# Kernel optimization log

Measured on AMD Instinct MI355X. Metric: run time of the kernel, lower is better.

Reference implementation:

```python
import jax, jax.numpy as jnp
import numpy as np

N_NODES = 100000
NUM_FEATURES = 512
HIDDEN = 128
OUT = 2
N_EDGES = 1600000


def setup_inputs() -> dict:
    key = jax.random.key(0)
    k_x, k_e, k_w1, k_b1, k_w2, k_b2 = jax.random.split(key, 6)
    x = jax.random.normal(k_x, (N_NODES, NUM_FEATURES), dtype=jnp.float32)
    edge_index = jax.random.randint(k_e, (2, N_EDGES), 0, N_NODES, dtype=jnp.int64)
    # GCNConv weight (Glorot-style scale) and bias
    w1 = jax.random.normal(k_w1, (NUM_FEATURES, HIDDEN), dtype=jnp.float32) / np.sqrt(NUM_FEATURES)
    b1 = jnp.zeros((HIDDEN,), dtype=jnp.float32)
    # nn.Linear weight/bias
    w2 = jax.random.normal(k_w2, (HIDDEN, OUT), dtype=jnp.float32) / np.sqrt(HIDDEN)
    b2 = jnp.zeros((OUT,), dtype=jnp.float32)
    return {"x": x, "w1": w1, "b1": b1, "w2": w2, "b2": b2, "edge_index": edge_index}


def _gcn_conv(x, edge_index, w, b, num_nodes):
    """PyG GCNConv: h = D^{-1/2} (A+I) D^{-1/2} (x @ w) + b."""
    h = x @ w  # [N, hidden] -- transform before propagate (PyG order)
    loops = jnp.arange(num_nodes, dtype=edge_index.dtype)
    src = jnp.concatenate([edge_index[0], loops])  # [E+N]
    dst = jnp.concatenate([edge_index[1], loops])
    # symmetric normalization: deg computed over destination (col) incl. self-loops
    deg = jnp.zeros((num_nodes,), dtype=h.dtype).at[dst].add(1.0)
    dinv = jax.lax.rsqrt(deg)  # deg >= 1 thanks to self-loops
    norm = dinv[src] * dinv[dst]  # [E+N]
    msg = h[src] * norm[:, None]  # gather + scale, [E+N, hidden]
    out = jax.ops.segment_sum(msg, dst, num_segments=num_nodes)  # scatter-add
    return out + b


def reference(x, w1, b1, w2, b2, edge_index):
    h = _gcn_conv(x, edge_index, w1, b1, N_NODES)  # [N, hidden]
    return h @ w2 + b2  # [N, out]
```

## Files before the change

### kernel.cpp

```cpp
#include <hip/hip_runtime.h>

constexpr int N_NODES = 100000;
constexpr int N_FEAT  = 512;
constexpr int N_EDGES = 1600000;

constexpr float FXS = 1048576.0f;
constexpr float FXB = 32.0f;

constexpr int BSH   = 8;
constexpr int BINW  = 1 << BSH;
constexpr int NBINS = (N_NODES + BINW - 1) >> BSH;
constexpr int BCAP  = 5120;
constexpr int NBB   = 128;
constexpr int CHUNK = N_EDGES / NBB;
constexpr int NRB   = 2048;

typedef float vfloat4 __attribute__((ext_vector_type(4)));

constexpr int WS_W    = 0;
constexpr int WS_C    = 1024;
constexpr int WS_CUR  = 1056;
constexpr int WS_DEG  = WS_CUR + 512;
constexpr int WS_DINV = WS_DEG + N_NODES;
constexpr int WS_G    = WS_DINV + N_NODES;
constexpr int WS_BINS = WS_G + 2 * N_NODES;

__global__ void k_prep(const float* __restrict__ w1, const float* __restrict__ w2,
                       const float* __restrict__ b1, const float* __restrict__ b2,
                       float* __restrict__ ws) {
    int i = blockIdx.x * blockDim.x + threadIdx.x;
    if (i < NBINS) reinterpret_cast<int*>(ws + WS_CUR)[i] = 0;
    if (i < N_FEAT) {
        float a0 = 0.f, a1 = 0.f;
        for (int m = 0; m < 128; ++m) {
            float w = w1[i * 128 + m];
            a0 += w * w2[m * 2 + 0];
            a1 += w * w2[m * 2 + 1];
        }
        ws[WS_W + i] = a0;
        ws[WS_W + 512 + i] = a1;
        if (i < 2) {
            float s = b2[i];
            for (int m = 0; m < 128; ++m) s += b1[m] * w2[m * 2 + i];
            ws[WS_C + i] = s;
        }
    }
}

__global__ __launch_bounds__(256) void k_fused(
    const float* __restrict__ x, float* __restrict__ ws,
    const int* __restrict__ src, const int* __restrict__ dst,
    float2* __restrict__ g) {
    int b = blockIdx.x;
    if (b < NBB) {
        __shared__ int cnt[NBINS];
        __shared__ int offs[NBINS];
        __shared__ int cur2[NBINS];
        int tid = threadIdx.x;
        for (int i = tid; i < NBINS; i += 256) { cnt[i] = 0; cur2[i] = 0; }
        __syncthreads();
        int base = b * CHUNK;
        for (int e = base + tid; e < base + CHUNK; e += 256)
            atomicAdd(&cnt[dst[e] >> BSH], 1);
        __syncthreads();
        int* gcur = reinterpret_cast<int*>(ws + WS_CUR);
        for (int i = tid; i < NBINS; i += 256) {
            int c = cnt[i];
            int pos = c ? atomicAdd(&gcur[i], c) : 0;
            offs[i] = i * BCAP + pos;
        }
        __syncthreads();
        unsigned int* bins = reinterpret_cast<unsigned int*>(ws + WS_BINS);
        for (int e = base + tid; e < base + CHUNK; e += 256) {
            int d = dst[e], s = src[e];
            int bin = d >> BSH;
            int r = atomicAdd(&cur2[bin], 1);
            bins[offs[bin] + r] = (unsigned int)s | ((unsigned int)(d & (BINW - 1)) << 17);
        }
        return;
    }
    int rb = b - NBB;
    const vfloat4* W0q = reinterpret_cast<const vfloat4*>(ws + WS_W);
    const vfloat4* W1q = reinterpret_cast<const vfloat4*>(ws + WS_W + 512);
    int lane = threadIdx.x & 63;
    int wave = threadIdx.x >> 6;

    vfloat4 w0a = W0q[lane], w0b = W0q[64 + lane];
    vfloat4 w1a = W1q[lane], w1b = W1q[64 + lane];

    int wid = rb * 4 + wave;
    int nw  = NRB * 4;
    constexpr int NPAIR = N_NODES / 2;
    for (int p = wid; p < NPAIR; p += nw) {
        int row0 = p * 2;
        const vfloat4* xq0 = reinterpret_cast<const vfloat4*>(x + (size_t)row0 * N_FEAT);
        const vfloat4* xq1 = xq0 + 128;
        vfloat4 xa = __builtin_nontemporal_load(&xq0[lane]);
        vfloat4 xb = __builtin_nontemporal_load(&xq0[64 + lane]);
        vfloat4 ya = __builtin_nontemporal_load(&xq1[lane]);
        vfloat4 yb = __builtin_nontemporal_load(&xq1[64 + lane]);
        float a0 = xa.x*w0a.x + xa.y*w0a.y + xa.z*w0a.z + xa.w*w0a.w
                 + xb.x*w0b.x + xb.y*w0b.y + xb.z*w0b.z + xb.w*w0b.w;
        float a1 = xa.x*w1a.x + xa.y*w1a.y + xa.z*w1a.z + xa.w*w1a.w
                 + xb.x*w1b.x + xb.y*w1b.y + xb.z*w1b.z + xb.w*w1b.w;
        float b0 = ya.x*w0a.x + ya.y*w0a.y + ya.z*w0a.z + ya.w*w0a.w
                 + yb.x*w0b.x + yb.y*w0b.y + yb.z*w0b.z + yb.w*w0b.w;
        float b1v= ya.x*w1a.x + ya.y*w1a.y + ya.z*w1a.z + ya.w*w1a.w
                 + yb.x*w1b.x + yb.y*w1b.y + yb.z*w1b.z + yb.w*w1b.w;
        #pragma unroll
        for (int off = 32; off >= 1; off >>= 1) {
            a0 += __shfl_down(a0, off);
            a1 += __shfl_down(a1, off);
            b0 += __shfl_down(b0, off);
            b1v+= __shfl_down(b1v, off);
        }
        if (lane == 0) {
            g[row0]     = make_float2(a0, a1);
            g[row0 + 1] = make_float2(b0, b1v);
        }
    }
}

__global__ __launch_bounds__(256) void k_deg(float* __restrict__ ws) {
    int b = blockIdx.x;
    const int* gcur = reinterpret_cast<const int*>(ws + WS_CUR);
    const unsigned int* bins = reinterpret_cast<const unsigned int*>(ws + WS_BINS) + b * BCAP;
    int n = min(gcur[b], BCAP);
    __shared__ int cnt[BINW];
    cnt[threadIdx.x] = 0;
    __syncthreads();
    for (int i = threadIdx.x; i < n; i += 256)
        atomicAdd(&cnt[bins[i] >> 17], 1);
    __syncthreads();
    int d = (b << BSH) + threadIdx.x;
    if (d < N_NODES) {
        int dg = cnt[threadIdx.x] + 1;
        reinterpret_cast<int*>(ws + WS_DEG)[d] = dg;
        ws[WS_DINV + d] = rsqrtf((float)dg);
    }
}

__global__ __launch_bounds__(256) void k_pass2(float* __restrict__ ws,
                                               float2* __restrict__ out) {
    int b = blockIdx.x;
    const int* gcur = reinterpret_cast<const int*>(ws + WS_CUR);
    const unsigned int* bins = reinterpret_cast<const unsigned int*>(ws + WS_BINS) + b * BCAP;
    const int* deg = reinterpret_cast<const int*>(ws + WS_DEG);
    const float* dinv = ws + WS_DINV;
    const float2* g = reinterpret_cast<const float2*>(ws + WS_G);
    int n = min(gcur[b], BCAP);
    __shared__ unsigned long long acc[BINW];
    acc[threadIdx.x] = 0ull;
    __syncthreads();
    for (int i = threadIdx.x; i < n; i += 256) {
        unsigned int p = bins[i];
        int s  = (int)(p & 0x1FFFFu);
        int ld = (int)(p >> 17);
        float2 gv = g[s];
        float di = dinv[s];
        unsigned int lo = (unsigned int)__float2int_rn((gv.x * di + FXB) * FXS);
        unsigned int hi = (unsigned int)__float2int_rn((gv.y * di + FXB) * FXS);
        atomicAdd(&acc[ld], ((unsigned long long)hi << 32) | (unsigned long long)lo);
    }
    __syncthreads();
    int d = (b << BSH) + threadIdx.x;
    if (d < N_NODES) {
        unsigned long long a = acc[threadIdx.x];
        long long cnt = (long long)(deg[d] - 1);
        long long bias = cnt << 25;
        long long lo = (long long)(a & 0xFFFFFFFFull) - bias;
        long long hi = (long long)(a >> 32) - bias;
        float di = dinv[d];
        float2 gv = g[d];
        float s0 = (float)lo * (1.0f / FXS) + gv.x * di;
        float s1 = (float)hi * (1.0f / FXS) + gv.y * di;
        out[d] = make_float2(di * s0 + ws[WS_C + 0], di * s1 + ws[WS_C + 1]);
    }
}

extern "C" void kernel_launch(void* const* d_in, const int* in_sizes, int n_in,
                              void* d_out, int out_size, void* d_ws, size_t ws_size,
                              hipStream_t stream) {
    const float* x  = (const float*)d_in[0];
    const float* w1 = (const float*)d_in[1];
    const float* b1 = (const float*)d_in[2];
    const float* w2 = (const float*)d_in[3];
    const float* b2 = (const float*)d_in[4];
    const int*   ei = (const int*)d_in[5];
    float* ws = (float*)d_ws;

    float2* g = (float2*)(ws + WS_G);

    k_prep<<<2, 256, 0, stream>>>(w1, w2, b1, b2, ws);
    k_fused<<<NBB + NRB, 256, 0, stream>>>(x, ws, ei, ei + N_EDGES, g);
    k_deg<<<NBINS, 256, 0, stream>>>(ws);
    k_pass2<<<NBINS, 256, 0, stream>>>(ws, (float2*)d_out);
}
```

Baseline: 90.66 us.

## Fold degree pass into binning blocks via grid barrier; restructure x-projection to 4 rows per wave

The separate degree kernel is removed. The 128 binning blocks now sync through a global atomic counter and then compute degree and dinv for their share of bins, which saves one kernel launch. The x @ W projection now has each wave handle 4 rows, with 16 lanes per row and 8 vector loads per lane. This cuts the shuffle reduction from 6 to 4 steps and gives each lane more loads in flight. The spin barrier depends on all 128 binning blocks being resident at the same time, which adds a risk of deadlock. The row-block count is also lowered.

```diff
diff --git a/kernel.cpp b/kernel.cpp
--- a/kernel.cpp
+++ b/kernel.cpp
@@ -13,7 +13,8 @@
 constexpr int BCAP  = 5120;
 constexpr int NBB   = 128;
 constexpr int CHUNK = N_EDGES / NBB;
-constexpr int NRB   = 2048;
+constexpr int NRB   = 1920;
+constexpr int GRID  = NBB + NRB;
 
 typedef float vfloat4 __attribute__((ext_vector_type(4)));
 
@@ -25,11 +26,13 @@
 constexpr int WS_G    = WS_DINV + N_NODES;
 constexpr int WS_BINS = WS_G + 2 * N_NODES;
 
+static_assert(N_NODES % 4 == 0, "");
+
 __global__ void k_prep(const float* __restrict__ w1, const float* __restrict__ w2,
                        const float* __restrict__ b1, const float* __restrict__ b2,
                        float* __restrict__ ws) {
     int i = blockIdx.x * blockDim.x + threadIdx.x;
-    if (i < NBINS) reinterpret_cast<int*>(ws + WS_CUR)[i] = 0;
+    if (i < NBINS + 1) reinterpret_cast<int*>(ws + WS_CUR)[i] = 0;
     if (i < N_FEAT) {
         float a0 = 0.f, a1 = 0.f;
         for (int m = 0; m < 128; ++m) {
@@ -47,10 +50,9 @@
     }
 }
 
-__global__ __launch_bounds__(256) void k_fused(
+__global__ __launch_bounds__(256) void k_main(
     const float* __restrict__ x, float* __restrict__ ws,
-    const int* __restrict__ src, const int* __restrict__ dst,
-    float2* __restrict__ g) {
+    const int* __restrict__ src, const int* __restrict__ dst) {
     int b = blockIdx.x;
     if (b < NBB) {
         __shared__ int cnt[NBINS];
@@ -77,66 +79,73 @@
             int r = atomicAdd(&cur2[bin], 1);
             bins[offs[bin] + r] = (unsigned int)s | ((unsigned int)(d & (BINW - 1)) << 17);
         }
+        __threadfence();
+        __syncthreads();
+        int* flag = gcur + NBINS;
+        if (tid == 0) {
+            __hip_atomic_fetch_add(flag, 1, __ATOMIC_ACQ_REL, __HIP_MEMORY_SCOPE_AGENT);
+            while (__hip_atomic_load(flag, __ATOMIC_ACQUIRE, __HIP_MEMORY_SCOPE_AGENT) < NBB)
+                __builtin_amdgcn_s_sleep(2);
+        }
+        __syncthreads();
+        __threadfence();
+        int* degp = reinterpret_cast<int*>(ws + WS_DEG);
+        for (int bin = b; bin < NBINS; bin += NBB) {
+            int n = __hip_atomic_load(&gcur[bin], __ATOMIC_RELAXED, __HIP_MEMORY_SCOPE_AGENT);
+            n = min(n, BCAP);
+            if (tid < BINW) cnt[tid] = 0;
+            __syncthreads();
+            const unsigned int* bb = bins + bin * BCAP;
+            for (int i = tid; i < n; i += 256)
+                atomicAdd(&cnt[bb[i] >> 17], 1);
+            __syncthreads();
+            int d = (bin << BSH) + tid;
+            if (tid < BINW && d < N_NODES) {
+                int dg = cnt[tid] + 1;
+                degp[d] = dg;
+                ws[WS_DINV + d] = rsqrtf((float)dg);
+            }
+            __syncthreads();
+        }
         return;
     }
     int rb = b - NBB;
     const vfloat4* W0q = reinterpret_cast<const vfloat4*>(ws + WS_W);
     const vfloat4* W1q = reinterpret_cast<const vfloat4*>(ws + WS_W + 512);
+    float2* g = reinterpret_cast<float2*>(ws + WS_G);
     int lane = threadIdx.x & 63;
     int wave = threadIdx.x >> 6;
-
-    vfloat4 w0a = W0q[lane], w0b = W0q[64 + lane];
-    vfloat4 w1a = W1q[lane], w1b = W1q[64 + lane];
+    int j = lane & 15, i4 = lane >> 4;
+
+    vfloat4 w0[8], w1[8];
+    #pragma unroll
+    for (int k = 0; k < 8; ++k) {
+        w0[k] = W0q[k * 16 + j];
+        w1[k] = W1q[k * 16 + j];
+    }
 
     int wid = rb * 4 + wave;
     int nw  = NRB * 4;
-    constexpr int NPAIR = N_NODES / 2;
-    for (int p = wid; p < NPAIR; p += nw) {
-        int row0 = p * 2;
-        const vfloat4* xq0 = reinterpret_cast<const vfloat4*>(x + (size_t)row0 * N_FEAT);
-        const vfloat4* xq1 = xq0 + 128;
-        vfloat4 xa = __builtin_nontemporal_load(&xq0[lane]);
-        vfloat4 xb = __builtin_nontemporal_load(&xq0[64 + lane]);
-        vfloat4 ya = __builtin_nontemporal_load(&xq1[lane]);
-        vfloat4 yb = __builtin_nontemporal_load(&xq1[64 + lane]);
-        float a0 = xa.x*w0a.x + xa.y*w0a.y + xa.z*w0a.z + xa.w*w0a.w
-                 + xb.x*w0b.x + xb.y*w0b.y + xb.z*w0b.z + xb.w*w0b.w;
-        float a1 = xa.x*w1a.x + xa.y*w1a.y + xa.z*w1a.z + xa.w*w1a.w
-                 + xb.x*w1b.x + xb.y*w1b.y + xb.z*w1b.z + xb.w*w1b.w;
-        float b0 = ya.x*w0a.x + ya.y*w0a.y + ya.z*w0a.z + ya.w*w0a.w
-                 + yb.x*w0b.x + yb.y*w0b.y + yb.z*w0b.z + yb.w*w0b.w;
-        float b1v= ya.x*w1a.x + ya.y*w1a.y + ya.z*w1a.z + ya.w*w1a.w
-                 + yb.x*w1b.x + yb.y*w1b.y + yb.z*w1b.z + yb.w*w1b.w;
+    constexpr int NQ = N_NODES / 4;
+    for (int q = wid; q < NQ; q += nw) {
+        int row = q * 4 + i4;
+        const vfloat4* xr = reinterpret_cast<const vfloat4*>(x + (size_t)row * N_FEAT);
+        vfloat4 xv[8];
         #pragma unroll
-        for (int off = 32; off >= 1; off >>= 1) {
-            a0 += __shfl_down(a0, off);
-            a1 += __shfl_down(a1, off);
-            b0 += __shfl_down(b0, off);
-            b1v+= __shfl_down(b1v, off);
-        }
-        if (lane == 0) {
-            g[row0]     = make_float2(a0, a1);
-            g[row0 + 1] = make_float2(b0, b1v);
-        }
-    }
-}
-
-__global__ __launch_bounds__(256) void k_deg(float* __restrict__ ws) {
-    int b = blockIdx.x;
-    const int* gcur = reinterpret_cast<const int*>(ws + WS_CUR);
-    const unsigned int* bins = reinterpret_cast<const unsigned int*>(ws + WS_BINS) + b * BCAP;
-    int n = min(gcur[b], BCAP);
-    __shared__ int cnt[BINW];
-    cnt[threadIdx.x] = 0;
-    __syncthreads();
-    for (int i = threadIdx.x; i < n; i += 256)
-        atomicAdd(&cnt[bins[i] >> 17], 1);
-    __syncthreads();
-    int d = (b << BSH) + threadIdx.x;
-    if (d < N_NODES) {
-        int dg = cnt[threadIdx.x] + 1;
-        reinterpret_cast<int*>(ws + WS_DEG)[d] = dg;
-        ws[WS_DINV + d] = rsqrtf((float)dg);
+        for (int k = 0; k < 8; ++k)
+            xv[k] = __builtin_nontemporal_load(&xr[k * 16 + j]);
+        float a0 = 0.f, a1 = 0.f;
+        #pragma unroll
+        for (int k = 0; k < 8; ++k) {
+            a0 += xv[k].x*w0[k].x + xv[k].y*w0[k].y + xv[k].z*w0[k].z + xv[k].w*w0[k].w;
+            a1 += xv[k].x*w1[k].x + xv[k].y*w1[k].y + xv[k].z*w1[k].z + xv[k].w*w1[k].w;
+        }
+        #pragma unroll
+        for (int off = 1; off <= 8; off <<= 1) {
+            a0 += __shfl_xor(a0, off);
+            a1 += __shfl_xor(a1, off);
+        }
+        if (j == 0) g[row] = make_float2(a0, a1);
     }
 }
 
@@ -166,8 +175,8 @@
     int d = (b << BSH) + threadIdx.x;
     if (d < N_NODES) {
         unsigned long long a = acc[threadIdx.x];
-        long long cnt = (long long)(deg[d] - 1);
-        long long bias = cnt << 25;
+        long long cntv = (long long)(deg[d] - 1);
+        long long bias = cntv << 25;
         long long lo = (long long)(a & 0xFFFFFFFFull) - bias;
         long long hi = (long long)(a >> 32) - bias;
         float di = dinv[d];
@@ -189,10 +198,7 @@
     const int*   ei = (const int*)d_in[5];
     float* ws = (float*)d_ws;
 
-    float2* g = (float2*)(ws + WS_G);
-
     k_prep<<<2, 256, 0, stream>>>(w1, w2, b1, b2, ws);
-    k_fused<<<NBB + NRB, 256, 0, stream>>>(x, ws, ei, ei + N_EDGES, g);
-    k_deg<<<NBINS, 256, 0, stream>>>(ws);
+    k_main<<<GRID, 256, 0, stream>>>(x, ws, ei, ei + N_EDGES);
     k_pass2<<<NBINS, 256, 0, stream>>>(ws, (float2*)d_out);
 }
```

Measured after the change: 139.1 us. 1.53x slower.
